# Performance work log

Hardware: AMD Instinct MI355X
Metric: run time of the kernel (lower is better)

## Reference

```python
import jax, jax.numpy as jnp
import numpy as np


def _lstm_scan(x_pre, h0, c0, W_hh, b_hh, reverse):
    """x_pre: [T,B,4H] precomputed input gates; h0,c0: [B,H].
    reverse=True processes right-to-left and returns outputs in original time order
    (equivalent to flip -> scan -> flip in the torch code)."""
    H = h0.shape[-1]

    def step(carry, g_in):
        h, c = carry
        gates = g_in + h @ W_hh.T + b_hh  # [B,4H]
        i, f, g, o = jnp.split(gates, 4, axis=-1)
        i = jax.nn.sigmoid(i)
        f = jax.nn.sigmoid(f)
        g = jnp.tanh(g)
        o = jax.nn.sigmoid(o)
        c = f * c + i * g
        h = o * jnp.tanh(c)
        return (h, c), h

    (h_T, c_T), ys = jax.lax.scan(step, (h0, c0), x_pre, reverse=reverse)
    return ys, h_T, c_T


def reference(x, h0, c0, W_ih, b_ih, W_hh, b_hh):
    # x: [T,B,D]; h0,c0: [2,B,H]; W_ih: [2,4H,D]; W_hh: [2,4H,H]; b_*: [2,4H]
    outs = []
    h_finals = []
    c_finals = []
    for d, rev in ((0, False), (1, True)):
        # precompute in2hidden over all timesteps: [T,B,4H]
        x_pre = jnp.einsum('tbd,gd->tbg', x, W_ih[d]) + b_ih[d]
        ys, h_T, c_T = _lstm_scan(x_pre, h0[d], c0[d], W_hh[d], b_hh[d], rev)
        outs.append(ys)
        h_finals.append(h_T)
        c_finals.append(c_T)
    output = jnp.concatenate(outs, axis=-1)          # [T,B,2H]
    h_out = jnp.stack(h_finals, axis=0)              # [2,B,H]
    c_out = jnp.stack(c_finals, axis=0)              # [2,B,H]
    return output, (h_out, c_out)


def setup_inputs() -> dict:
    key = jax.random.key(0)
    ks = jax.random.split(key, 7)
    T, B, D, H = 512, 32, 512, 512
    s = 1.0 / np.sqrt(H)
    return {
        'x': jax.random.normal(ks[0], (T, B, D), dtype=jnp.float32),
        'h0': jax.random.normal(ks[1], (2, B, H), dtype=jnp.float32),
        'c0': jax.random.normal(ks[2], (2, B, H), dtype=jnp.float32),
        'W_ih': jax.random.normal(ks[3], (2, 4 * H, D), dtype=jnp.float32) * s,
        'b_ih': jax.random.normal(ks[4], (2, 4 * H), dtype=jnp.float32) * s,
        'W_hh': jax.random.normal(ks[5], (2, 4 * H, H), dtype=jnp.float32) * s,
        'b_hh': jax.random.normal(ks[6], (2, 4 * H), dtype=jnp.float32) * s,
    }
```

## Files before the change

### kernel.cpp

```cpp
#include <hip/hip_runtime.h>

#define TT    512
#define BB    32
#define HH    512
#define NBDIR 128
#define NTHR_R 128

typedef __attribute__((ext_vector_type(8))) short short8;
typedef __attribute__((ext_vector_type(4))) float f32x4;
typedef __attribute__((ext_vector_type(4))) unsigned u32x4;
typedef __attribute__((ext_vector_type(2))) unsigned u32x2;

#define SELH 0x05040100u
#define SELL 0x07060302u

__device__ __forceinline__ ushort bf16_rne(float v) {
    unsigned u = __builtin_bit_cast(unsigned, v);
    unsigned r = u + 0x7FFFu + ((u >> 16) & 1u);
    return (ushort)(r >> 16);
}
__device__ __forceinline__ float bf16_to_f(ushort h) {
    unsigned u = ((unsigned)h) << 16;
    return __builtin_bit_cast(float, u);
}

__device__ __forceinline__ u32x4 ld_cohere_x4(const unsigned* p) {
    u32x4 r;
    asm volatile("global_load_dwordx4 %0, %1, off sc0 sc1" : "=v"(r) : "v"(p) : "memory");
    return r;
}
__device__ __forceinline__ unsigned ld_plain_x1(const unsigned* p) {
    unsigned r;
    asm volatile("global_load_dword %0, %1, off" : "=v"(r) : "v"(p) : "memory");
    return r;
}
#define WAIT_VM(N) do { asm volatile("s_waitcnt vmcnt(" #N ")" ::: "memory"); \
                        __builtin_amdgcn_sched_barrier(0); } while (0)

__device__ __forceinline__ void unpack8(const u32x4& A, const u32x4& B,
                                        short8& hi, short8& lo) {
    u32x4 h = { __builtin_amdgcn_perm(A[1], A[0], SELH), __builtin_amdgcn_perm(A[3], A[2], SELH),
                __builtin_amdgcn_perm(B[1], B[0], SELH), __builtin_amdgcn_perm(B[3], B[2], SELH) };
    u32x4 l = { __builtin_amdgcn_perm(A[1], A[0], SELL), __builtin_amdgcn_perm(A[3], A[2], SELL),
                __builtin_amdgcn_perm(B[1], B[0], SELL), __builtin_amdgcn_perm(B[3], B[2], SELL) };
    hi = __builtin_bit_cast(short8, h);
    lo = __builtin_bit_cast(short8, l);
}

__global__ void __launch_bounds__(256, 1)
xpre_gemm(const float* __restrict__ x, const float* __restrict__ W_ih,
          unsigned* __restrict__ XP, unsigned* __restrict__ flags) {
    __shared__ __align__(16) char sA[32768];
    __shared__ __align__(16) char sB[32768];
    const int tid = threadIdx.x;
    const int bid = blockIdx.x;
    if (bid == 0) flags[tid] = 0u;
    const int d  = bid & 1;
    const int nt = (bid >> 1) & 15;
    const int mt = bid >> 5;
    const int lane = tid & 63, wid = tid >> 6;
    const int wm = wid >> 1, wn = wid & 1;
    const int lr = lane & 15, lk8 = (lane >> 4) * 8;

    f32x4 acc[16];
    #pragma unroll
    for (int i = 0; i < 16; ++i) acc[i] = (f32x4){0.f, 0.f, 0.f, 0.f};

    const float* Ab = x + (size_t)(mt * 128) * 512;
    const float* Bb = W_ih + ((size_t)d * 2048 + nt * 128) * 512;

    for (int kc = 0; kc < 8; ++kc) {
        #pragma unroll
        for (int i = 0; i < 8; ++i) {
            int f = i * 256 + tid;
            int row = f >> 4, fc = f & 15;
            int byte = (row * 128 + fc * 8) ^ ((row & 7) << 4);
            f32x4 va = *(const f32x4*)(Ab + (size_t)row * 512 + kc * 64 + fc * 4);
            f32x4 vb = *(const f32x4*)(Bb + (size_t)row * 512 + kc * 64 + fc * 4);
            ushort h0 = bf16_rne(va[0]), h1 = bf16_rne(va[1]), h2 = bf16_rne(va[2]), h3 = bf16_rne(va[3]);
            ushort l0 = bf16_rne(va[0] - bf16_to_f(h0)), l1 = bf16_rne(va[1] - bf16_to_f(h1));
            ushort l2 = bf16_rne(va[2] - bf16_to_f(h2)), l3 = bf16_rne(va[3] - bf16_to_f(h3));
            *(u32x2*)(sA + byte)         = (u32x2){ (unsigned)h0 | ((unsigned)h1 << 16),
                                                    (unsigned)h2 | ((unsigned)h3 << 16) };
            *(u32x2*)(sA + 16384 + byte) = (u32x2){ (unsigned)l0 | ((unsigned)l1 << 16),
                                                    (unsigned)l2 | ((unsigned)l3 << 16) };
            h0 = bf16_rne(vb[0]); h1 = bf16_rne(vb[1]); h2 = bf16_rne(vb[2]); h3 = bf16_rne(vb[3]);
            l0 = bf16_rne(vb[0] - bf16_to_f(h0)); l1 = bf16_rne(vb[1] - bf16_to_f(h1));
            l2 = bf16_rne(vb[2] - bf16_to_f(h2)); l3 = bf16_rne(vb[3] - bf16_to_f(h3));
            *(u32x2*)(sB + byte)         = (u32x2){ (unsigned)h0 | ((unsigned)h1 << 16),
                                                    (unsigned)h2 | ((unsigned)h3 << 16) };
            *(u32x2*)(sB + 16384 + byte) = (u32x2){ (unsigned)l0 | ((unsigned)l1 << 16),
                                                    (unsigned)l2 | ((unsigned)l3 << 16) };
        }
        __syncthreads();
        #pragma unroll
        for (int ks = 0; ks < 2; ++ks) {
            short8 bh[4], bl[4];
            #pragma unroll
            for (int ns = 0; ns < 4; ++ns) {
                int brow = wn * 64 + ns * 16 + lr;
                int byte = (brow * 128 + (ks * 32 + lk8) * 2) ^ ((brow & 7) << 4);
                bh[ns] = *(const short8*)(sB + byte);
                bl[ns] = *(const short8*)(sB + 16384 + byte);
            }
            #pragma unroll
            for (int ms = 0; ms < 4; ++ms) {
                int arow = wm * 64 + ms * 16 + lr;
                int byte = (arow * 128 + (ks * 32 + lk8) * 2) ^ ((arow & 7) << 4);
                short8 ah = *(const short8*)(sA + byte);
                short8 al = *(const short8*)(sA + 16384 + byte);
                #pragma unroll
                for (int ns = 0; ns < 4; ++ns) {
                    acc[ms*4+ns] = __builtin_amdgcn_mfma_f32_16x16x32_bf16(ah, bh[ns], acc[ms*4+ns], 0,0,0);
                    acc[ms*4+ns] = __builtin_amdgcn_mfma_f32_16x16x32_bf16(al, bh[ns], acc[ms*4+ns], 0,0,0);
                    acc[ms*4+ns] = __builtin_amdgcn_mfma_f32_16x16x32_bf16(ah, bl[ns], acc[ms*4+ns], 0,0,0);
                }
            }
        }
        __syncthreads();
    }
    #pragma unroll
    for (int ms = 0; ms < 4; ++ms)
    #pragma unroll
    for (int ns = 0; ns < 4; ++ns)
    #pragma unroll
    for (int r = 0; r < 4; ++r) {
        float v = acc[ms*4+ns][r];
        int m = mt * 128 + wm * 64 + ms * 16 + (lane >> 4) * 4 + r;
        int n = nt * 128 + wn * 64 + ns * 16 + lr;
        int t = m >> 5, b = m & 31;
        int q = n >> 9, rem = n & 511, bk = rem >> 2, jl = rem & 3;
        ushort hi = bf16_rne(v);
        ushort lo = bf16_rne(v - bf16_to_f(hi));
        XP[((((size_t)d * 128 + bk) * 512 + t) * 32 + b) * 16 + (q * 4 + jl)] =
            (unsigned)hi | ((unsigned)lo << 16);
    }
}

__global__ void __launch_bounds__(NTHR_R, 1)
lstm_persist(const float* __restrict__ h0, const float* __restrict__ c0,
             const float* __restrict__ W_hh, const float* __restrict__ b_ih,
             const float* __restrict__ b_hh, const unsigned* __restrict__ XP,
             unsigned* __restrict__ h_buf, unsigned* __restrict__ flags,
             float* __restrict__ out) {
    __shared__ __align__(16) char sW[32768];
    __shared__ float sC[32][17];
    __shared__ float sBias[16];

    const int tid = threadIdx.x, bid = blockIdx.x;
    const int d = bid >> 7, blk = bid & 127, j0 = blk * 4;

    for (int idx = tid; idx < 16 * 512; idx += NTHR_R) {
        int r = idx >> 9, col = idx & 511;
        int g = (r >> 2) * 512 + j0 + (r & 3);
        float v = W_hh[((size_t)d * 2048 + g) * 512 + col];
        ushort hi = bf16_rne(v), lo = bf16_rne(v - bf16_to_f(hi));
        int byte = (r * 1024 + col * 2) ^ ((r & 7) << 4);
        *(ushort*)(sW + byte)         = hi;
        *(ushort*)(sW + 16384 + byte) = lo;
    }
    if (tid < 16) {
        int g = (tid >> 2) * 512 + j0 + (tid & 3);
        sBias[tid] = b_ih[d * 2048 + g] + b_hh[d * 2048 + g];
    }

    const int b_own = tid >> 2, jl_own = tid & 3, j_own = j0 + jl_own;
    float c_reg = c0[(d * BB + b_own) * HH + j_own];
    float h_reg = h0[(d * BB + b_own) * HH + j_own];
    {
        ushort hi = bf16_rne(h_reg), lo = bf16_rne(h_reg - bf16_to_f(hi));
        __hip_atomic_store(h_buf + (0 * 2 + d) * 16384 + b_own * HH + j_own,
                           (unsigned)hi | ((unsigned)lo << 16),
                           __ATOMIC_RELAXED, __HIP_MEMORY_SCOPE_AGENT);
    }
    __syncthreads();
    if (tid == 0)
        __hip_atomic_store(flags + d * NBDIR + blk, 1u,
                           __ATOMIC_RELAXED, __HIP_MEMORY_SCOPE_AGENT);

    const int lane = tid & 63, w = tid >> 6;
    const int lr = lane & 15, lk8 = (lane >> 4) * 8;
    unsigned* fl = flags + d * NBDIR;

    for (int s = 0; s < TT; ++s) {
        const int t_eff = d ? (TT - 1 - s) : s;
        const int p = s & 1;

        const unsigned* xpb = XP + (((size_t)d * 128 + blk) * 512 + t_eff) * 512;
        unsigned xr0 = ld_plain_x1(xpb + (w * 16 + (lane >> 4) * 4 + 0) * 16 + lr);
        unsigned xr1 = ld_plain_x1(xpb + (w * 16 + (lane >> 4) * 4 + 1) * 16 + lr);
        unsigned xr2 = ld_plain_x1(xpb + (w * 16 + (lane >> 4) * 4 + 2) * 16 + lr);
        unsigned xr3 = ld_plain_x1(xpb + (w * 16 + (lane >> 4) * 4 + 3) * 16 + lr);

        if (tid < 64) {
            unsigned tgt = (unsigned)s + 1u;
            for (;;) {
                unsigned a = __hip_atomic_load(fl + tid,      __ATOMIC_RELAXED, __HIP_MEMORY_SCOPE_AGENT);
                unsigned b = __hip_atomic_load(fl + 64 + tid, __ATOMIC_RELAXED, __HIP_MEMORY_SCOPE_AGENT);
                if (__all(a >= tgt && b >= tgt)) break;
                __builtin_amdgcn_s_sleep(1);
            }
        }
        __syncthreads();
        WAIT_VM(0);

        const unsigned* hb = h_buf + (p * 2 + d) * 16384 + (w * 16 + lr) * HH;
        u32x4 A0[8], A1[8];
        f32x4 acc = {0.f, 0.f, 0.f, 0.f};

        auto issue_kb = [&](u32x4 (&buf)[8], int kb) {
            #pragma unroll
            for (int i = 0; i < 4; ++i) {
                const unsigned* pp = hb + kb * 128 + i * 32 + lk8;
                buf[2*i]   = ld_cohere_x4(pp);
                buf[2*i+1] = ld_cohere_x4(pp + 4);
            }
        };
        auto do_kb = [&](u32x4 (&buf)[8], int kb) {
            #pragma unroll
            for (int i = 0; i < 4; ++i) {
                short8 ah, al;
                unpack8(buf[2*i], buf[2*i+1], ah, al);
                int byte = (lr * 1024 + (kb * 128 + i * 32 + lk8) * 2) ^ ((lr & 7) << 4);
                short8 bh = *(const short8*)(sW + byte);
                short8 bl = *(const short8*)(sW + 16384 + byte);
                acc = __builtin_amdgcn_mfma_f32_16x16x32_bf16(ah, bh, acc, 0, 0, 0);
                acc = __builtin_amdgcn_mfma_f32_16x16x32_bf16(al, bh, acc, 0, 0, 0);
                acc = __builtin_amdgcn_mfma_f32_16x16x32_bf16(ah, bl, acc, 0, 0, 0);
            }
        };

        issue_kb(A0, 0);
        issue_kb(A1, 1);
        WAIT_VM(8);  do_kb(A0, 0);
        issue_kb(A0, 2);
        WAIT_VM(8);  do_kb(A1, 1);
        issue_kb(A1, 3);
        WAIT_VM(8);  do_kb(A0, 2);
        WAIT_VM(0);  do_kb(A1, 3);

        {
            float xf0 = bf16_to_f((ushort)(xr0 & 0xFFFF)) + bf16_to_f((ushort)(xr0 >> 16));
            float xf1 = bf16_to_f((ushort)(xr1 & 0xFFFF)) + bf16_to_f((ushort)(xr1 >> 16));
            float xf2 = bf16_to_f((ushort)(xr2 & 0xFFFF)) + bf16_to_f((ushort)(xr2 >> 16));
            float xf3 = bf16_to_f((ushort)(xr3 & 0xFFFF)) + bf16_to_f((ushort)(xr3 >> 16));
            int row = w * 16 + (lane >> 4) * 4;
            sC[row + 0][lr] = acc[0] + xf0;
            sC[row + 1][lr] = acc[1] + xf1;
            sC[row + 2][lr] = acc[2] + xf2;
            sC[row + 3][lr] = acc[3] + xf3;
        }
        __syncthreads();

        float gi = sC[b_own][ 0 + jl_own] + sBias[ 0 + jl_own];
        float gf = sC[b_own][ 4 + jl_own] + sBias[ 4 + jl_own];
        float gg = sC[b_own][ 8 + jl_own] + sBias[ 8 + jl_own];
        float go = sC[b_own][12 + jl_own] + sBias[12 + jl_own];
        float ig = 1.f / (1.f + expf(-gi));
        float fg = 1.f / (1.f + expf(-gf));
        float gt = tanhf(gg);
        float og = 1.f / (1.f + expf(-go));
        c_reg = fg * c_reg + ig * gt;
        h_reg = og * tanhf(c_reg);

        out[(t_eff * BB + b_own) * 1024 + d * 512 + j_own] = h_reg;
        {
            ushort hi = bf16_rne(h_reg), lo = bf16_rne(h_reg - bf16_to_f(hi));
            __hip_atomic_store(h_buf + ((p ^ 1) * 2 + d) * 16384 + b_own * HH + j_own,
                               (unsigned)hi | ((unsigned)lo << 16),
                               __ATOMIC_RELAXED, __HIP_MEMORY_SCOPE_AGENT);
        }
        __syncthreads();
        if (tid == 0)
            __hip_atomic_store(flags + d * NBDIR + blk, (unsigned)s + 2u,
                               __ATOMIC_RELAXED, __HIP_MEMORY_SCOPE_AGENT);
    }

    out[16777216 +         (d * BB + b_own) * HH + j_own] = h_reg;
    out[16777216 + 32768 + (d * BB + b_own) * HH + j_own] = c_reg;
}

extern "C" void kernel_launch(void* const* d_in, const int* in_sizes, int n_in,
                              void* d_out, int out_size, void* d_ws, size_t ws_size,
                              hipStream_t stream) {
    const float* x    = (const float*)d_in[0];
    const float* h0   = (const float*)d_in[1];
    const float* c0   = (const float*)d_in[2];
    const float* W_ih = (const float*)d_in[3];
    const float* b_ih = (const float*)d_in[4];
    const float* W_hh = (const float*)d_in[5];
    const float* b_hh = (const float*)d_in[6];
    float* out = (float*)d_out;

    unsigned* XP    = (unsigned*)d_ws;
    unsigned* h_buf = XP + (size_t)2 * 128 * 512 * 32 * 16;
    unsigned* flags = h_buf + 4 * 16384;

    xpre_gemm<<<4096, 256, 0, stream>>>(x, W_ih, XP, flags);

    void* args[] = { &h0, &c0, &W_hh, &b_ih, &b_hh, &XP, &h_buf, &flags, &out };
    hipLaunchCooperativeKernel((void*)lstm_persist, dim3(2 * NBDIR), dim3(NTHR_R),
                               args, 0, stream);
}
```

Baseline: 3.162 ms.

## Replace flag barrier with key-tagged hidden-state polling and halve recurrent blocks

Removes the per-step flag array and block barrier. Each hidden value is now stored with a step-dependent check word (payload XOR key), and consumers poll the data itself until every tag matches, so each MFMA sub-chunk can start as soon as its own slice arrives. Blocks per direction drop from 128 to 64, each covering 8 hidden units, with double the LDS weights and a reordered XP layout loaded as vectors. This cuts the number of synchronising blocks and the flag round-trip, but doubles the per-block recurrent MFMA work and the bytes read for h.

```diff
diff --git a/kernel.cpp b/kernel.cpp
--- a/kernel.cpp
+++ b/kernel.cpp
@@ -3,7 +3,7 @@
 #define TT    512
 #define BB    32
 #define HH    512
-#define NBDIR 128
+#define NBDIR 64
 #define NTHR_R 128
 
 typedef __attribute__((ext_vector_type(8))) short short8;
@@ -13,6 +13,7 @@
 
 #define SELH 0x05040100u
 #define SELL 0x07060302u
+#define GOLD 0x9E3779B9u
 
 __device__ __forceinline__ ushort bf16_rne(float v) {
     unsigned u = __builtin_bit_cast(unsigned, v);
@@ -24,37 +25,49 @@
     return __builtin_bit_cast(float, u);
 }
 
-__device__ __forceinline__ u32x4 ld_cohere_x4(const unsigned* p) {
-    u32x4 r;
-    asm volatile("global_load_dwordx4 %0, %1, off sc0 sc1" : "=v"(r) : "v"(p) : "memory");
-    return r;
-}
-__device__ __forceinline__ unsigned ld_plain_x1(const unsigned* p) {
-    unsigned r;
-    asm volatile("global_load_dword %0, %1, off" : "=v"(r) : "v"(p) : "memory");
-    return r;
-}
+__device__ __forceinline__ unsigned keyof(int s) { return (unsigned)(s + 1) * GOLD; }
+
+#define LDT(dst, PB, OFF) \
+    asm volatile("global_load_dwordx4 %0, %1, off offset:%c2 sc0 sc1" \
+                 : "=v"(dst) : "v"(PB), "i"(OFF) : "memory")
+#define LDP4(dst, P) \
+    asm volatile("global_load_dwordx4 %0, %1, off" : "=v"(dst) : "v"(P) : "memory")
 #define WAIT_VM(N) do { asm volatile("s_waitcnt vmcnt(" #N ")" ::: "memory"); \
                         __builtin_amdgcn_sched_barrier(0); } while (0)
 
-__device__ __forceinline__ void unpack8(const u32x4& A, const u32x4& B,
-                                        short8& hi, short8& lo) {
-    u32x4 h = { __builtin_amdgcn_perm(A[1], A[0], SELH), __builtin_amdgcn_perm(A[3], A[2], SELH),
-                __builtin_amdgcn_perm(B[1], B[0], SELH), __builtin_amdgcn_perm(B[3], B[2], SELH) };
-    u32x4 l = { __builtin_amdgcn_perm(A[1], A[0], SELL), __builtin_amdgcn_perm(A[3], A[2], SELL),
-                __builtin_amdgcn_perm(B[1], B[0], SELL), __builtin_amdgcn_perm(B[3], B[2], SELL) };
-    hi = __builtin_bit_cast(short8, h);
-    lo = __builtin_bit_cast(short8, l);
+#define ISSUE_SUB(BUF, PB, SB) do { \
+    LDT(BUF[0], PB, (SB)*512+  0); LDT(BUF[1], PB, (SB)*512+ 16); \
+    LDT(BUF[2], PB, (SB)*512+ 32); LDT(BUF[3], PB, (SB)*512+ 48); \
+    LDT(BUF[4], PB, (SB)*512+256); LDT(BUF[5], PB, (SB)*512+272); \
+    LDT(BUF[6], PB, (SB)*512+288); LDT(BUF[7], PB, (SB)*512+304); \
+} while (0)
+
+__device__ __forceinline__ bool sub_ok(const u32x4* buf, unsigned key) {
+    unsigned bad = 0u;
+    #pragma unroll
+    for (int i = 0; i < 8; ++i)
+        bad |= (buf[i][0] ^ buf[i][1] ^ key) | (buf[i][2] ^ buf[i][3] ^ key);
+    return __all((bad == 0u) ? 1 : 0) != 0;
+}
+#define POLL_SUB(BUF, PB, SB, KEY) \
+    while (!sub_ok(BUF, KEY)) { __builtin_amdgcn_s_sleep(1); \
+        ISSUE_SUB(BUF, PB, SB); WAIT_VM(0); }
+
+__device__ __forceinline__ void st_tag2(unsigned* p, unsigned pay, unsigned chk) {
+    u32x2 v = { pay, chk };
+    asm volatile("global_store_dwordx2 %0, %1, off sc0 sc1" :: "v"(p), "v"(v) : "memory");
+}
+__device__ __forceinline__ void st_f(float* p, float v) {
+    asm volatile("global_store_dword %0, %1, off" :: "v"(p), "v"(v) : "memory");
 }
 
 __global__ void __launch_bounds__(256, 1)
 xpre_gemm(const float* __restrict__ x, const float* __restrict__ W_ih,
-          unsigned* __restrict__ XP, unsigned* __restrict__ flags) {
+          unsigned* __restrict__ XP) {
     __shared__ __align__(16) char sA[32768];
     __shared__ __align__(16) char sB[32768];
     const int tid = threadIdx.x;
     const int bid = blockIdx.x;
-    if (bid == 0) flags[tid] = 0u;
     const int d  = bid & 1;
     const int nt = (bid >> 1) & 15;
     const int mt = bid >> 5;
@@ -129,10 +142,10 @@
         int m = mt * 128 + wm * 64 + ms * 16 + (lane >> 4) * 4 + r;
         int n = nt * 128 + wn * 64 + ns * 16 + lr;
         int t = m >> 5, b = m & 31;
-        int q = n >> 9, rem = n & 511, bk = rem >> 2, jl = rem & 3;
+        int q = n >> 9, rem = n & 511, bk = rem >> 3, jl = rem & 7;
         ushort hi = bf16_rne(v);
         ushort lo = bf16_rne(v - bf16_to_f(hi));
-        XP[((((size_t)d * 128 + bk) * 512 + t) * 32 + b) * 16 + (q * 4 + jl)] =
+        XP[((((size_t)d * 64 + bk) * 512 + t) * 32 + b) * 32 + (jl * 4 + q)] =
             (unsigned)hi | ((unsigned)lo << 16);
     }
 }
@@ -141,143 +154,157 @@
 lstm_persist(const float* __restrict__ h0, const float* __restrict__ c0,
              const float* __restrict__ W_hh, const float* __restrict__ b_ih,
              const float* __restrict__ b_hh, const unsigned* __restrict__ XP,
-             unsigned* __restrict__ h_buf, unsigned* __restrict__ flags,
-             float* __restrict__ out) {
-    __shared__ __align__(16) char sW[32768];
-    __shared__ float sC[32][17];
-    __shared__ float sBias[16];
+             unsigned* __restrict__ h_tag, float* __restrict__ out) {
+    __shared__ __align__(16) char sW[65536];
+    __shared__ float sC[32][33];
+    __shared__ float sBias[32];
 
     const int tid = threadIdx.x, bid = blockIdx.x;
-    const int d = bid >> 7, blk = bid & 127, j0 = blk * 4;
-
-    for (int idx = tid; idx < 16 * 512; idx += NTHR_R) {
+    const int d = bid >> 6, blk = bid & 63, j0 = blk * 8;
+
+    for (int idx = tid; idx < 32 * 512; idx += NTHR_R) {
         int r = idx >> 9, col = idx & 511;
-        int g = (r >> 2) * 512 + j0 + (r & 3);
+        int jl = r >> 2, q = r & 3, g = q * 512 + j0 + jl;
         float v = W_hh[((size_t)d * 2048 + g) * 512 + col];
         ushort hi = bf16_rne(v), lo = bf16_rne(v - bf16_to_f(hi));
         int byte = (r * 1024 + col * 2) ^ ((r & 7) << 4);
         *(ushort*)(sW + byte)         = hi;
-        *(ushort*)(sW + 16384 + byte) = lo;
-    }
-    if (tid < 16) {
-        int g = (tid >> 2) * 512 + j0 + (tid & 3);
+        *(ushort*)(sW + 32768 + byte) = lo;
+    }
+    if (tid < 32) {
+        int jl = tid >> 2, q = tid & 3, g = q * 512 + j0 + jl;
         sBias[tid] = b_ih[d * 2048 + g] + b_hh[d * 2048 + g];
     }
 
-    const int b_own = tid >> 2, jl_own = tid & 3, j_own = j0 + jl_own;
-    float c_reg = c0[(d * BB + b_own) * HH + j_own];
-    float h_reg = h0[(d * BB + b_own) * HH + j_own];
-    {
-        ushort hi = bf16_rne(h_reg), lo = bf16_rne(h_reg - bf16_to_f(hi));
-        __hip_atomic_store(h_buf + (0 * 2 + d) * 16384 + b_own * HH + j_own,
-                           (unsigned)hi | ((unsigned)lo << 16),
-                           __ATOMIC_RELAXED, __HIP_MEMORY_SCOPE_AGENT);
+    const int b_own = tid >> 2, jl_own = tid & 3;
+    float c_reg[2], h_reg[2];
+    #pragma unroll
+    for (int v = 0; v < 2; ++v) {
+        int j = j0 + jl_own + v * 4;
+        c_reg[v] = c0[(d * BB + b_own) * HH + j];
+        h_reg[v] = h0[(d * BB + b_own) * HH + j];
+        ushort hi = bf16_rne(h_reg[v]), lo = bf16_rne(h_reg[v] - bf16_to_f(hi));
+        unsigned pay = (unsigned)hi | ((unsigned)lo << 16);
+        st_tag2(h_tag + ((size_t)(0 * 2 + d) * 32 + b_own) * 1024 + j * 2,
+                pay, pay ^ keyof(0));
     }
     __syncthreads();
-    if (tid == 0)
-        __hip_atomic_store(flags + d * NBDIR + blk, 1u,
-                           __ATOMIC_RELAXED, __HIP_MEMORY_SCOPE_AGENT);
 
     const int lane = tid & 63, w = tid >> 6;
     const int lr = lane & 15, lk8 = (lane >> 4) * 8;
-    unsigned* fl = flags + d * NBDIR;
+    const int brow = w * 16 + lr;
+
+    u32x4 A[8], B[8];
 
     for (int s = 0; s < TT; ++s) {
         const int t_eff = d ? (TT - 1 - s) : s;
         const int p = s & 1;
-
-        const unsigned* xpb = XP + (((size_t)d * 128 + blk) * 512 + t_eff) * 512;
-        unsigned xr0 = ld_plain_x1(xpb + (w * 16 + (lane >> 4) * 4 + 0) * 16 + lr);
-        unsigned xr1 = ld_plain_x1(xpb + (w * 16 + (lane >> 4) * 4 + 1) * 16 + lr);
-        unsigned xr2 = ld_plain_x1(xpb + (w * 16 + (lane >> 4) * 4 + 2) * 16 + lr);
-        unsigned xr3 = ld_plain_x1(xpb + (w * 16 + (lane >> 4) * 4 + 3) * 16 + lr);
-
-        if (tid < 64) {
-            unsigned tgt = (unsigned)s + 1u;
-            for (;;) {
-                unsigned a = __hip_atomic_load(fl + tid,      __ATOMIC_RELAXED, __HIP_MEMORY_SCOPE_AGENT);
-                unsigned b = __hip_atomic_load(fl + 64 + tid, __ATOMIC_RELAXED, __HIP_MEMORY_SCOPE_AGENT);
-                if (__all(a >= tgt && b >= tgt)) break;
-                __builtin_amdgcn_s_sleep(1);
+        const unsigned key  = keyof(s);
+        const unsigned nkey = keyof(s + 1);
+
+        const unsigned* xpb =
+            XP + ((((size_t)d * 64 + blk) * 512 + t_eff) * 32 + b_own) * 32;
+        u32x4 xpA, xpB;
+        LDP4(xpA, xpb + jl_own * 4);
+        LDP4(xpB, xpb + (jl_own + 4) * 4);
+
+        const unsigned* pb =
+            h_tag + ((size_t)(p * 2 + d) * 32 + brow) * 1024 + lk8 * 2;
+
+        f32x4 acc0 = {0.f, 0.f, 0.f, 0.f}, acc1 = acc0;
+
+        auto mfma_sub = [&](const u32x4* buf, int sb) {
+            #pragma unroll
+            for (int ksl = 0; ksl < 2; ++ksl) {
+                unsigned p0 = buf[ksl*4+0][0], p1 = buf[ksl*4+0][2];
+                unsigned p2 = buf[ksl*4+1][0], p3 = buf[ksl*4+1][2];
+                unsigned p4 = buf[ksl*4+2][0], p5 = buf[ksl*4+2][2];
+                unsigned p6 = buf[ksl*4+3][0], p7 = buf[ksl*4+3][2];
+                u32x4 hh = { __builtin_amdgcn_perm(p1, p0, SELH), __builtin_amdgcn_perm(p3, p2, SELH),
+                             __builtin_amdgcn_perm(p5, p4, SELH), __builtin_amdgcn_perm(p7, p6, SELH) };
+                u32x4 ll = { __builtin_amdgcn_perm(p1, p0, SELL), __builtin_amdgcn_perm(p3, p2, SELL),
+                             __builtin_amdgcn_perm(p5, p4, SELL), __builtin_amdgcn_perm(p7, p6, SELL) };
+                short8 ah = __builtin_bit_cast(short8, hh);
+                short8 al = __builtin_bit_cast(short8, ll);
+                int k2 = (sb * 64 + ksl * 32 + lk8) * 2;
+                {   int byte = (lr * 1024 + k2) ^ ((lr & 7) << 4);
+                    short8 bh = *(const short8*)(sW + byte);
+                    short8 bl = *(const short8*)(sW + 32768 + byte);
+                    acc0 = __builtin_amdgcn_mfma_f32_16x16x32_bf16(ah, bh, acc0, 0,0,0);
+                    acc0 = __builtin_amdgcn_mfma_f32_16x16x32_bf16(al, bh, acc0, 0,0,0);
+                    acc0 = __builtin_amdgcn_mfma_f32_16x16x32_bf16(ah, bl, acc0, 0,0,0);
+                }
+                {   int srow = 16 + lr;
+                    int byte = (srow * 1024 + k2) ^ ((srow & 7) << 4);
+                    short8 bh = *(const short8*)(sW + byte);
+                    short8 bl = *(const short8*)(sW + 32768 + byte);
+                    acc1 = __builtin_amdgcn_mfma_f32_16x16x32_bf16(ah, bh, acc1, 0,0,0);
+                    acc1 = __builtin_amdgcn_mfma_f32_16x16x32_bf16(al, bh, acc1, 0,0,0);
+                    acc1 = __builtin_amdgcn_mfma_f32_16x16x32_bf16(ah, bl, acc1, 0,0,0);
+                }
             }
+        };
+
+        ISSUE_SUB(A, pb, 0);
+        ISSUE_SUB(B, pb, 1);
+        WAIT_VM(8); POLL_SUB(A, pb, 0, key); mfma_sub(A, 0);
+        ISSUE_SUB(A, pb, 2);
+        WAIT_VM(8); POLL_SUB(B, pb, 1, key); mfma_sub(B, 1);
+        ISSUE_SUB(B, pb, 3);
+        WAIT_VM(8); POLL_SUB(A, pb, 2, key); mfma_sub(A, 2);
+        ISSUE_SUB(A, pb, 4);
+        WAIT_VM(8); POLL_SUB(B, pb, 3, key); mfma_sub(B, 3);
+        ISSUE_SUB(B, pb, 5);
+        WAIT_VM(8); POLL_SUB(A, pb, 4, key); mfma_sub(A, 4);
+        ISSUE_SUB(A, pb, 6);
+        WAIT_VM(8); POLL_SUB(B, pb, 5, key); mfma_sub(B, 5);
+        ISSUE_SUB(B, pb, 7);
+        WAIT_VM(8); POLL_SUB(A, pb, 6, key); mfma_sub(A, 6);
+        WAIT_VM(0); POLL_SUB(B, pb, 7, key); mfma_sub(B, 7);
+
+        #pragma unroll
+        for (int r = 0; r < 4; ++r) {
+            int row = w * 16 + (lane >> 4) * 4 + r;
+            sC[row][lr]      = acc0[r];
+            sC[row][16 + lr] = acc1[r];
         }
         __syncthreads();
-        WAIT_VM(0);
-
-        const unsigned* hb = h_buf + (p * 2 + d) * 16384 + (w * 16 + lr) * HH;
-        u32x4 A0[8], A1[8];
-        f32x4 acc = {0.f, 0.f, 0.f, 0.f};
-
-        auto issue_kb = [&](u32x4 (&buf)[8], int kb) {
-            #pragma unroll
-            for (int i = 0; i < 4; ++i) {
-                const unsigned* pp = hb + kb * 128 + i * 32 + lk8;
-                buf[2*i]   = ld_cohere_x4(pp);
-                buf[2*i+1] = ld_cohere_x4(pp + 4);
-            }
-        };
-        auto do_kb = [&](u32x4 (&buf)[8], int kb) {
-            #pragma unroll
-            for (int i = 0; i < 4; ++i) {
-                short8 ah, al;
-                unpack8(buf[2*i], buf[2*i+1], ah, al);
-                int byte = (lr * 1024 + (kb * 128 + i * 32 + lk8) * 2) ^ ((lr & 7) << 4);
-                short8 bh = *(const short8*)(sW + byte);
-                short8 bl = *(const short8*)(sW + 16384 + byte);
-                acc = __builtin_amdgcn_mfma_f32_16x16x32_bf16(ah, bh, acc, 0, 0, 0);
-                acc = __builtin_amdgcn_mfma_f32_16x16x32_bf16(al, bh, acc, 0, 0, 0);
-                acc = __builtin_amdgcn_mfma_f32_16x16x32_bf16(ah, bl, acc, 0, 0, 0);
-            }
-        };
-
-        issue_kb(A0, 0);
-        issue_kb(A1, 1);
-        WAIT_VM(8);  do_kb(A0, 0);
-        issue_kb(A0, 2);
-        WAIT_VM(8);  do_kb(A1, 1);
-        issue_kb(A1, 3);
-        WAIT_VM(8);  do_kb(A0, 2);
-        WAIT_VM(0);  do_kb(A1, 3);
-
-        {
-            float xf0 = bf16_to_f((ushort)(xr0 & 0xFFFF)) + bf16_to_f((ushort)(xr0 >> 16));
-            float xf1 = bf16_to_f((ushort)(xr1 & 0xFFFF)) + bf16_to_f((ushort)(xr1 >> 16));
-            float xf2 = bf16_to_f((ushort)(xr2 & 0xFFFF)) + bf16_to_f((ushort)(xr2 >> 16));
-            float xf3 = bf16_to_f((ushort)(xr3 & 0xFFFF)) + bf16_to_f((ushort)(xr3 >> 16));
-            int row = w * 16 + (lane >> 4) * 4;
-            sC[row + 0][lr] = acc[0] + xf0;
-            sC[row + 1][lr] = acc[1] + xf1;
-            sC[row + 2][lr] = acc[2] + xf2;
-            sC[row + 3][lr] = acc[3] + xf3;
+
+        const int pn = (s + 1) & 1;
+        #pragma unroll
+        for (int v = 0; v < 2; ++v) {
+            int jl = jl_own + v * 4;
+            u32x4 xp = v ? xpB : xpA;
+            float gi = sC[b_own][jl*4+0] + sBias[jl*4+0]
+                     + bf16_to_f((ushort)(xp[0] & 0xFFFF)) + bf16_to_f((ushort)(xp[0] >> 16));
+            float gf = sC[b_own][jl*4+1] + sBias[jl*4+1]
+                     + bf16_to_f((ushort)(xp[1] & 0xFFFF)) + bf16_to_f((ushort)(xp[1] >> 16));
+            float gg = sC[b_own][jl*4+2] + sBias[jl*4+2]
+                     + bf16_to_f((ushort)(xp[2] & 0xFFFF)) + bf16_to_f((ushort)(xp[2] >> 16));
+            float go = sC[b_own][jl*4+3] + sBias[jl*4+3]
+                     + bf16_to_f((ushort)(xp[3] & 0xFFFF)) + bf16_to_f((ushort)(xp[3] >> 16));
+            float ig = 1.f / (1.f + expf(-gi));
+            float fg = 1.f / (1.f + expf(-gf));
+            float gt = tanhf(gg);
+            float og = 1.f / (1.f + expf(-go));
+            c_reg[v] = fg * c_reg[v] + ig * gt;
+            h_reg[v] = og * tanhf(c_reg[v]);
+
+            int j = j0 + jl;
+            ushort hi = bf16_rne(h_reg[v]), lo = bf16_rne(h_reg[v] - bf16_to_f(hi));
+            unsigned pay = (unsigned)hi | ((unsigned)lo << 16);
+            st_tag2(h_tag + ((size_t)(pn * 2 + d) * 32 + b_own) * 1024 + j * 2,
+                    pay, pay ^ nkey);
+            st_f(out + ((size_t)t_eff * BB + b_own) * 1024 + d * 512 + j, h_reg[v]);
         }
-        __syncthreads();
-
-        float gi = sC[b_own][ 0 + jl_own] + sBias[ 0 + jl_own];
-        float gf = sC[b_own][ 4 + jl_own] + sBias[ 4 + jl_own];
-        float gg = sC[b_own][ 8 + jl_own] + sBias[ 8 + jl_own];
-        float go = sC[b_own][12 + jl_own] + sBias[12 + jl_own];
-        float ig = 1.f / (1.f + expf(-gi));
-        float fg = 1.f / (1.f + expf(-gf));
-        float gt = tanhf(gg);
-        float og = 1.f / (1.f + expf(-go));
-        c_reg = fg * c_reg + ig * gt;
-        h_reg = og * tanhf(c_reg);
-
-        out[(t_eff * BB + b_own) * 1024 + d * 512 + j_own] = h_reg;
-        {
-            ushort hi = bf16_rne(h_reg), lo = bf16_rne(h_reg - bf16_to_f(hi));
-            __hip_atomic_store(h_buf + ((p ^ 1) * 2 + d) * 16384 + b_own * HH + j_own,
-                               (unsigned)hi | ((unsigned)lo << 16),
-                               __ATOMIC_RELAXED, __HIP_MEMORY_SCOPE_AGENT);
-        }
-        __syncthreads();
-        if (tid == 0)
-            __hip_atomic_store(flags + d * NBDIR + blk, (unsigned)s + 2u,
-                               __ATOMIC_RELAXED, __HIP_MEMORY_SCOPE_AGENT);
-    }
-
-    out[16777216 +         (d * BB + b_own) * HH + j_own] = h_reg;
-    out[16777216 + 32768 + (d * BB + b_own) * HH + j_own] = c_reg;
+    }
+
+    #pragma unroll
+    for (int v = 0; v < 2; ++v) {
+        int j = j0 + jl_own + v * 4;
+        out[16777216 +         (d * BB + b_own) * HH + j] = h_reg[v];
+        out[16777216 + 32768 + (d * BB + b_own) * HH + j] = c_reg[v];
+    }
 }
 
 extern "C" void kernel_launch(void* const* d_in, const int* in_sizes, int n_in,
@@ -293,12 +320,11 @@
     float* out = (float*)d_out;
 
     unsigned* XP    = (unsigned*)d_ws;
-    unsigned* h_buf = XP + (size_t)2 * 128 * 512 * 32 * 16;
-    unsigned* flags = h_buf + 4 * 16384;
-
-    xpre_gemm<<<4096, 256, 0, stream>>>(x, W_ih, XP, flags);
-
-    void* args[] = { &h0, &c0, &W_hh, &b_ih, &b_hh, &XP, &h_buf, &flags, &out };
+    unsigned* h_tag = XP + (size_t)2 * 64 * 512 * 32 * 32;
+
+    xpre_gemm<<<4096, 256, 0, stream>>>(x, W_ih, XP);
+
+    void* args[] = { &h0, &c0, &W_hh, &b_ih, &b_hh, &XP, &h_tag, &out };
     hipLaunchCooperativeKernel((void*)lstm_persist, dim3(2 * NBDIR), dim3(NTHR_R),
                                args, 0, stream);
 }
```

Measured after the change: 4.684 ms. 48.1% more time.
